# Optimization experiments

Hardware: AMD Instinct MI355X
Metric: run time of the kernel (lower is better)

## Reference

```python
import jax, jax.numpy as jnp
import numpy as np

D_MODEL = 1024
D_STATE = 64
D_CONV = 4
EXPAND = 2
HEADDIM = 64
D_INNER = EXPAND * D_MODEL            # 2048
NHEADS = D_INNER // HEADDIM           # 32
CONV_DIM = D_INNER + 2 * D_STATE      # 2176
D_IN_PROJ = 2 * D_INNER + 2 * D_STATE + NHEADS  # 4256
B, L = 2, 1024


def _mamba2(x, in_proj_w, conv_w, conv_b, dt_bias, A_log, D_param, rms_w, out_proj_w):
    b, l, _ = x.shape
    zxbcdt = x @ in_proj_w.T                                   # (b,l,4256)
    z, xBC, dt = jnp.split(zxbcdt, [D_INNER, D_INNER + CONV_DIM], axis=-1)
    dt = jax.nn.softplus(dt + dt_bias)                         # (b,l,h)
    # depthwise causal conv over sequence
    xBC = jax.lax.conv_general_dilated(
        xBC, conv_w, (1,), [(D_CONV - 1, 0)],
        dimension_numbers=("NLC", "LIO", "NLC"),
        feature_group_count=CONV_DIM) + conv_b
    xBC = jax.nn.silu(xBC)
    xs, Bmat, Cmat = jnp.split(xBC, [D_INNER, D_INNER + D_STATE], axis=-1)
    xh = xs.reshape(b, l, NHEADS, HEADDIM)
    A = -jnp.exp(A_log)                                        # (h,)
    dA = jnp.exp(dt * A)                                       # (b,l,h)

    def step(h, inp):
        dA_t, dt_t, B_t, C_t, x_t = inp                        # (b,h),(b,h),(b,n),(b,n),(b,h,p)
        h = h * dA_t[..., None, None] + (dt_t[..., None] * x_t)[..., None] * B_t[:, None, None, :]
        y_t = jnp.einsum("bhpn,bn->bhp", h, C_t)
        return h, y_t

    h0 = jnp.zeros((b, NHEADS, HEADDIM, D_STATE), x.dtype)
    inps = (dA.transpose(1, 0, 2), dt.transpose(1, 0, 2),
            Bmat.transpose(1, 0, 2), Cmat.transpose(1, 0, 2),
            xh.transpose(1, 0, 2, 3))
    _, ys = jax.lax.scan(step, h0, inps)                       # (l,b,h,p)
    y = ys.transpose(1, 0, 2, 3) + D_param[None, None, :, None] * xh
    y = y.reshape(b, l, D_INNER)
    # gated RMSNorm (norm after gating, as in mamba_ssm RMSNormGated)
    y = y * jax.nn.silu(z)
    y = y * jax.lax.rsqrt(jnp.mean(y * y, axis=-1, keepdims=True) + 1e-5) * rms_w
    return y @ out_proj_w.T


def setup_inputs() -> dict:
    key = jax.random.key(0)
    ks = jax.random.split(key, 16)
    s = 0.02

    def mamba_params(i):
        kk = jax.random.split(ks[i], 8)
        dt = jnp.exp(jax.random.uniform(kk[4], (NHEADS,)) * (np.log(0.1) - np.log(1e-3)) + np.log(1e-3))
        dt_bias = dt + jnp.log(-jnp.expm1(-dt))
        return dict(
            in_proj_w=jax.random.normal(kk[0], (D_IN_PROJ, D_MODEL)) * s,
            conv_w=jax.random.normal(kk[1], (D_CONV, 1, CONV_DIM)) * 0.2,
            conv_b=jnp.zeros((CONV_DIM,)),
            dt_bias=dt_bias,
            A_log=jnp.log(jax.random.uniform(kk[2], (NHEADS,), minval=1.0, maxval=16.0)),
            D=jnp.ones((NHEADS,)),
            rms_w=jnp.ones((D_INNER,)),
            out_proj_w=jax.random.normal(kk[3], (D_MODEL, D_INNER)) * s,
        )

    pf = mamba_params(1)
    pb = mamba_params(2)
    inp = {"x": jax.random.normal(ks[0], (B, L, D_MODEL))}
    for name, v in pf.items():
        inp["f_" + name] = v
    for name, v in pb.items():
        inp["b_" + name] = v
    inp["proj_w"] = jax.random.normal(ks[3], (D_MODEL, 2 * D_MODEL)) * s
    inp["proj_b"] = jnp.zeros((D_MODEL,))
    inp["ln_w"] = jnp.ones((D_MODEL,))
    inp["ln_b"] = jnp.zeros((D_MODEL,))
    return inp


def reference(x, f_in_proj_w, f_conv_w, f_conv_b, f_dt_bias, f_A_log, f_D, f_rms_w, f_out_proj_w,
              b_in_proj_w, b_conv_w, b_conv_b, b_dt_bias, b_A_log, b_D, b_rms_w, b_out_proj_w,
              proj_w, proj_b, ln_w, ln_b):
    out_fwd = _mamba2(x, f_in_proj_w, f_conv_w, f_conv_b, f_dt_bias, f_A_log, f_D, f_rms_w, f_out_proj_w)
    out_bwd = _mamba2(jnp.flip(x, 1), b_in_proj_w, b_conv_w, b_conv_b, b_dt_bias, b_A_log, b_D, b_rms_w, b_out_proj_w)
    out_bwd = jnp.flip(out_bwd, 1)
    combined = jnp.concatenate([out_fwd, out_bwd], axis=-1)
    h = x + combined @ proj_w.T + proj_b
    mu = jnp.mean(h, axis=-1, keepdims=True)
    var = jnp.mean((h - mu) ** 2, axis=-1, keepdims=True)
    return (h - mu) * jax.lax.rsqrt(var + 1e-5) * ln_w + ln_b
```

## Files before the change

kernel.cpp:

```cpp
#include <hip/hip_runtime.h>
#include <hip/hip_bf16.h>

#define DEV __device__ __forceinline__

typedef short bf16x8 __attribute__((ext_vector_type(8)));
typedef float f32x4 __attribute__((ext_vector_type(4)));

static constexpr int BATCH  = 2;
static constexpr int SEQ    = 1024;
static constexpr int DMODEL = 1024;
static constexpr int DINNER = 2048;
static constexpr int DSTATE = 64;
static constexpr int NH     = 32;
static constexpr int HD     = 64;
static constexpr int CONVD  = 2176;
static constexpr int DPROJ  = 4256;
static constexpr int MROWS  = BATCH * SEQ;
static constexpr int NCHUNK = 16;
static constexpr int QC     = 64;

static constexpr size_t OFF_ZX = 0;
static constexpr size_t OFF_XS = OFF_ZX + (size_t)2*MROWS*DPROJ*2;
static constexpr size_t OFF_BB = OFF_XS + (size_t)2*MROWS*DINNER*2;
static constexpr size_t OFF_CC = OFF_BB + (size_t)2*MROWS*DSTATE*4;
static constexpr size_t OFF_DT = OFF_CC + (size_t)2*MROWS*DSTATE*4;
static constexpr size_t OFF_DA = OFF_DT + (size_t)2*MROWS*NH*4;
static constexpr size_t OFF_DR = OFF_DA + (size_t)2*MROWS*NH*4;
static constexpr size_t OFF_CS = OFF_DR + (size_t)2*MROWS*NH*4;
static constexpr size_t OFF_WO = OFF_CS;
static constexpr size_t OFF_WP = OFF_CS + (size_t)2*DMODEL*DINNER*2;
static constexpr size_t OFF_DD = 0;
static constexpr size_t OFF_H  = OFF_DD + (size_t)MROWS*2*DMODEL;

DEV float b2f(ushort u) {
    union { unsigned int i; float f; } v;
    v.i = ((unsigned int)u) << 16;
    return v.f;
}
DEV ushort f2b(float f) {
    union { float f; unsigned int u; } v;
    v.f = f;
    unsigned int r = 0x7FFFu + ((v.u >> 16) & 1u);
    return (ushort)((v.u + r) >> 16);
}
DEV bf16x8 pack8(float4 a, float4 b) {
    bf16x8 r;
    r[0] = (short)f2b(a.x); r[1] = (short)f2b(a.y);
    r[2] = (short)f2b(a.z); r[3] = (short)f2b(a.w);
    r[4] = (short)f2b(b.x); r[5] = (short)f2b(b.y);
    r[6] = (short)f2b(b.z); r[7] = (short)f2b(b.w);
    return r;
}
DEV void gll16(const ushort* g, ushort* l) {
    __builtin_amdgcn_global_load_lds(
        (const __attribute__((address_space(1))) unsigned int*)g,
        (__attribute__((address_space(3))) unsigned int*)l, 16, 0, 0);
}
DEV int idmap128(int bx) {
    int x8 = bx & 7, g = bx >> 3;
    return (x8 & 3) * 32 + (x8 >> 2) * 16 + g;
}

__global__ __launch_bounds__(256) void cvt3_k(
    const float* __restrict__ s0, const float* __restrict__ s1,
    const float* __restrict__ s2,
    ushort* __restrict__ d0, ushort* __restrict__ d1, ushort* __restrict__ d2,
    int b0, int b1)
{
    int blk = blockIdx.x;
    const float* s; ushort* d; size_t off;
    if (blk < b0)            { s = s0; d = d0; off = (size_t)blk * 1024; }
    else if (blk < b0 + b1)  { s = s1; d = d1; off = (size_t)(blk - b0) * 1024; }
    else                     { s = s2; d = d2; off = (size_t)(blk - b0 - b1) * 1024; }
    size_t i = off + threadIdx.x * 4;
    float4 f = *(const float4*)(s + i);
    ushort4 u;
    u.x = f2b(f.x); u.y = f2b(f.y); u.z = f2b(f.z); u.w = f2b(f.w);
    *(ushort4*)(d + i) = u;
}

template<int MODE, int BN, int BK>
__global__ __launch_bounds__(256) void gemm_k(
    const ushort* __restrict__ A, const ushort* __restrict__ W,
    size_t wstride, void* __restrict__ outp, const float* __restrict__ resid,
    const float* __restrict__ bias, float* __restrict__ dtraw,
    int N, int K)
{
    constexpr int BM = 128;
    constexpr int MT = (BN == 128) ? 4 : 2;
    constexpr int NSL = BK / 8;
    constexpr int RPG = 64 / NSL;
    constexpr int NAG = BM / RPG / 4;
    constexpr int NBG = BN / RPG / 4;
    __shared__ ushort As[BM * BK];
    __shared__ ushort Bs[BN * BK];
    const int tid = threadIdx.x;
    const int wave = tid >> 6, lane = tid & 63;
    const int quad = lane >> 4, l16 = lane & 15;
    const int bxu = (MODE == 0)
        ? (int)((blockIdx.x + 2 * blockIdx.y) % gridDim.x) : (int)blockIdx.x;
    const int bn = bxu * BN, bm = blockIdx.y * BM;
    const int dir = blockIdx.z;
    const ushort* Wd = W + (size_t)dir * wstride;
    const int wmoff = (BN == 128) ? (wave >> 1) * 64 : wave * 32;
    const int wnoff = (BN == 128) ? (wave & 1) * 64 : 0;

    const int lrow = lane / NSL, lslot = lane % NSL;
    const ushort* aga[NAG];
    ushort* ald[NAG];
    #pragma unroll
    for (int t = 0; t < NAG; t++) {
        int li = wave * NAG + t;
        int absr = li * RPG + lrow;
        int m = bm + absr;
        size_t rowidx;
        if (MODE == 0) {
            int b = m >> 10, l = m & 1023;
            int ls = dir ? (1023 - l) : l;
            rowidx = (size_t)((b << 10) + ls);
        } else if (MODE == 1) {
            rowidx = (size_t)(dir * MROWS + m);
        } else {
            rowidx = (size_t)m;
        }
        aga[t] = A + rowidx * K + (lslot ^ (absr % NSL)) * 8;
        ald[t] = &As[li * 512];
    }
    const ushort* bga[NBG];
    ushort* bld[NBG];
    #pragma unroll
    for (int t = 0; t < NBG; t++) {
        int li = wave * NBG + t;
        int absr = li * RPG + lrow;
        int n = bn + absr;
        if (n >= N) n = N - 1;
        bga[t] = Wd + (size_t)n * K + (lslot ^ (absr % NSL)) * 8;
        bld[t] = &Bs[li * 512];
    }

    f32x4 acc[MT][4] = {};

    for (int k0 = 0; k0 < K; k0 += BK) {
        #pragma unroll
        for (int t = 0; t < NAG; t++) gll16(aga[t] + k0, ald[t]);
        #pragma unroll
        for (int t = 0; t < NBG; t++) gll16(bga[t] + k0, bld[t]);
        __syncthreads();

        #pragma unroll
        for (int kt = 0; kt < BK / 32; kt++) {
            const int rs = (((kt * 4 + quad) ^ (l16 % NSL))) * 8;
            bf16x8 af[MT], bfr[4];
            #pragma unroll
            for (int mt = 0; mt < MT; mt++)
                af[mt] = *(const bf16x8*)&As[(wmoff + mt * 16 + l16) * BK + rs];
            #pragma unroll
            for (int nt = 0; nt < 4; nt++)
                bfr[nt] = *(const bf16x8*)&Bs[(wnoff + nt * 16 + l16) * BK + rs];
            #pragma unroll
            for (int mt = 0; mt < MT; mt++)
                #pragma unroll
                for (int nt = 0; nt < 4; nt++)
                    acc[mt][nt] = __builtin_amdgcn_mfma_f32_16x16x32_bf16(
                        af[mt], bfr[nt], acc[mt][nt], 0, 0, 0);
        }
        __syncthreads();
    }

    #pragma unroll
    for (int mt = 0; mt < MT; mt++) {
        #pragma unroll
        for (int nt = 0; nt < 4; nt++) {
            #pragma unroll
            for (int j = 0; j < 4; j++) {
                int row = bm + wmoff + mt * 16 + quad * 4 + j;
                int col = bn + wnoff + nt * 16 + l16;
                if (col >= N) continue;
                float v = acc[mt][nt][j];
                if (MODE == 0) {
                    ((ushort*)outp)[(size_t)(dir * MROWS + row) * DPROJ + col] = f2b(v);
                    if (col >= 4224)
                        dtraw[(size_t)(dir * MROWS + row) * NH + (col - 4224)] = v;
                } else if (MODE == 1) {
                    int mr = dir ? ((row & 1024) | (1023 - (row & 1023))) : row;
                    ((ushort*)outp)[(size_t)mr * (2 * DMODEL) + dir * DMODEL + col] = f2b(v);
                } else {
                    float r = resid[(size_t)row * DMODEL + col] + bias[col];
                    ((float*)outp)[(size_t)row * DMODEL + col] = v + r;
                }
            }
        }
    }
}

__global__ __launch_bounds__(256) void conv_k(
    const ushort* __restrict__ zx, const float* __restrict__ dtr,
    const float* __restrict__ cw0, const float* __restrict__ cb0,
    const float* __restrict__ cw1, const float* __restrict__ cb1,
    const float* __restrict__ dtb0, const float* __restrict__ al0,
    const float* __restrict__ dtb1, const float* __restrict__ al1,
    ushort* __restrict__ xs, float* __restrict__ Bq, float* __restrict__ Cq,
    float* __restrict__ dtq, float* __restrict__ ldq)
{
    int bx = blockIdx.x;
    int id = (bx & 7) * 512 + (bx >> 3);
    int dir = id >> 11;
    int m = id & 2047;
    int l = m & 1023;
    const float* cw = dir ? cw1 : cw0;
    const float* cb = dir ? cb1 : cb0;
    int tid = threadIdx.x;

    for (int c = tid * 4; c < CONVD; c += 1024) {
        float4 cbv = *(const float4*)&cb[c];
        float acc[4] = { cbv.x, cbv.y, cbv.z, cbv.w };
        #pragma unroll
        for (int t = 0; t < 4; t++) {
            int ls = l - 3 + t;
            if (ls >= 0) {
                float4 wv = *(const float4*)&cw[t * CONVD + c];
                ushort4 xv = *(const ushort4*)&zx[(size_t)(id - l + ls) * DPROJ + 2048 + c];
                acc[0] += wv.x * b2f(xv.x);
                acc[1] += wv.y * b2f(xv.y);
                acc[2] += wv.z * b2f(xv.z);
                acc[3] += wv.w * b2f(xv.w);
            }
        }
        float v[4];
        #pragma unroll
        for (int i = 0; i < 4; i++) v[i] = acc[i] / (1.f + expf(-acc[i]));
        if (c < DINNER) {
            ushort4 u;
            u.x = f2b(v[0]); u.y = f2b(v[1]); u.z = f2b(v[2]); u.w = f2b(v[3]);
            *(ushort4*)&xs[(size_t)id * DINNER + c] = u;
        } else if (c < DINNER + DSTATE) {
            *(float4*)&Bq[(size_t)id * DSTATE + (c - DINNER)] =
                make_float4(v[0], v[1], v[2], v[3]);
        } else {
            *(float4*)&Cq[(size_t)id * DSTATE + (c - DINNER - DSTATE)] =
                make_float4(v[0], v[1], v[2], v[3]);
        }
    }
    if (tid < NH) {
        const float* dtb = dir ? dtb1 : dtb0;
        const float* al  = dir ? al1 : al0;
        float raw = dtr[(size_t)id * NH + tid] + dtb[tid];
        float dt = raw > 20.f ? raw : log1pf(expf(raw));
        float ldA = -expf(al[tid]) * dt;
        int dirb = id >> 10;
        dtq[(size_t)(dirb * NH + tid) * SEQ + l] = dt;
        ldq[(size_t)(dirb * NH + tid) * SEQ + l] = ldA;
    }
}

__global__ __launch_bounds__(256) void states_k(
    const float* __restrict__ Bq, const float* __restrict__ dtT,
    const float* __restrict__ ldT, const ushort* __restrict__ xsq,
    ushort* __restrict__ cs)
{
    int id = idmap128(blockIdx.x);
    int h = id & 31;
    int c = blockIdx.y;
    int tid = threadIdx.x;
    int wave = tid >> 6, lane = tid & 63;
    int quad = lane >> 4;
    int base = (id >> 5) << 10;
    int l0 = c * QC;

    __shared__ float wsh[QC];
    __shared__ ushort Xw[64][80];
    __shared__ ushort Bt[64][72];

    if (tid < 64) {
        float ld = ldT[(size_t)id * SEQ + l0 + tid];
        #pragma unroll
        for (int st = 1; st < 64; st <<= 1) {
            float o = __shfl_up(ld, st);
            if (tid >= st) ld += o;
        }
        float tot = __shfl(ld, 63);
        wsh[tid] = dtT[(size_t)id * SEQ + l0 + tid] * expf(tot - ld);
    }
    __syncthreads();

    {
        int j = tid >> 2, p0 = (tid & 3) * 16;
        float wj = wsh[j];
        const ushort* xrow = xsq + (size_t)(base + l0 + j) * DINNER + h * HD + p0;
        #pragma unroll
        for (int q = 0; q < 4; q++) {
            ushort4 xv = *(const ushort4*)(xrow + q * 4);
            Xw[p0 + q * 4 + 0][j] = f2b(b2f(xv.x) * wj);
            Xw[p0 + q * 4 + 1][j] = f2b(b2f(xv.y) * wj);
            Xw[p0 + q * 4 + 2][j] = f2b(b2f(xv.z) * wj);
            Xw[p0 + q * 4 + 3][j] = f2b(b2f(xv.w) * wj);
        }
        int j2 = lane, ng = wave * 16;
        const float* brow = Bq + (size_t)(base + l0 + j2) * DSTATE + ng;
        #pragma unroll
        for (int q = 0; q < 4; q++) {
            float4 f = *(const float4*)(brow + q * 4);
            Bt[ng + q * 4 + 0][j2] = f2b(f.x);
            Bt[ng + q * 4 + 1][j2] = f2b(f.y);
            Bt[ng + q * 4 + 2][j2] = f2b(f.z);
            Bt[ng + q * 4 + 3][j2] = f2b(f.w);
        }
    }
    __syncthreads();

    f32x4 acc[4] = {};
    #pragma unroll
    for (int kt = 0; kt < 2; kt++) {
        int k = kt * 32 + quad * 8;
        bf16x8 af = *(const bf16x8*)&Xw[wave * 16 + (lane & 15)][k];
        #pragma unroll
        for (int ni = 0; ni < 4; ni++) {
            bf16x8 bf = *(const bf16x8*)&Bt[ni * 16 + (lane & 15)][k];
            acc[ni] = __builtin_amdgcn_mfma_f32_16x16x32_bf16(af, bf, acc[ni], 0, 0, 0);
        }
    }

    ushort* out = cs + ((size_t)id * NCHUNK + c) * HD * DSTATE;
    #pragma unroll
    for (int ni = 0; ni < 4; ni++) {
        #pragma unroll
        for (int j = 0; j < 4; j++) {
            int p = wave * 16 + quad * 4 + j;
            int n = ni * 16 + (lane & 15);
            out[(size_t)p * DSTATE + n] = f2b(acc[ni][j]);
        }
    }
}

__global__ __launch_bounds__(256) void stitch_k(
    const float* __restrict__ ldT, ushort* __restrict__ cs)
{
    int id = blockIdx.x;
    int tid = threadIdx.x;
    __shared__ float red[256];
    __shared__ float dec[NCHUNK];

    float4 d4 = *(const float4*)(ldT + (size_t)id * SEQ + tid * 4);
    red[tid] = d4.x + d4.y + d4.z + d4.w;
    __syncthreads();
    if (tid < NCHUNK) {
        float s = 0.f;
        #pragma unroll
        for (int i = 0; i < 16; i++) s += red[tid * 16 + i];
        dec[tid] = expf(s);
    }
    __syncthreads();

    int p = tid >> 2, n0 = (tid & 3) * 16;
    ushort* ptr = cs + (size_t)id * NCHUNK * HD * DSTATE + p * DSTATE + n0;

    float st[16];
    #pragma unroll
    for (int i = 0; i < 16; i++) st[i] = 0.f;

    for (int c = 0; c < NCHUNK; c++) {
        ushort* row = ptr + (size_t)c * HD * DSTATE;
        float tmp[16];
        #pragma unroll
        for (int i = 0; i < 16; i++) tmp[i] = b2f(row[i]);
        #pragma unroll
        for (int i = 0; i < 16; i++) row[i] = f2b(st[i]);
        float d = dec[c];
        #pragma unroll
        for (int i = 0; i < 16; i++) st[i] = fmaf(d, st[i], tmp[i]);
    }
}

__global__ __launch_bounds__(256) void ssd_k(
    const float* __restrict__ Bq, const float* __restrict__ Cq,
    const float* __restrict__ dtT, const float* __restrict__ ldT,
    const ushort* __restrict__ xsq, const ushort* __restrict__ cs,
    const float* __restrict__ D0, const float* __restrict__ D1,
    ushort* __restrict__ yout)
{
    int id = idmap128(blockIdx.x);
    int dir = id >> 6, h = id & 31;
    int c = blockIdx.y;
    int tid = threadIdx.x;
    int wave = tid >> 6, lane = tid & 63;
    int quad = lane >> 4;
    int base = (id >> 5) << 10;
    int l0 = c * QC;

    __shared__ float cum[QC], dts[QC];
    __shared__ ushort Ms[64][72];
    __shared__ ushort Xb[64][80];

    {
        int j = tid >> 2, p0 = (tid & 3) * 16;
        const ushort* xrow = xsq + (size_t)(base + l0 + j) * DINNER + h * HD + p0;
        #pragma unroll
        for (int q = 0; q < 4; q++) {
            ushort4 xv = *(const ushort4*)(xrow + q * 4);
            Xb[p0 + q * 4 + 0][j] = xv.x;
            Xb[p0 + q * 4 + 1][j] = xv.y;
            Xb[p0 + q * 4 + 2][j] = xv.z;
            Xb[p0 + q * 4 + 3][j] = xv.w;
        }
    }
    if (tid < 64) {
        float ld = ldT[(size_t)id * SEQ + l0 + tid];
        #pragma unroll
        for (int st = 1; st < 64; st <<= 1) {
            float o = __shfl_up(ld, st);
            if (tid >= st) ld += o;
        }
        cum[tid] = ld;
        dts[tid] = dtT[(size_t)id * SEQ + l0 + tid];
    }

    f32x4 sacc[4] = {};
    #pragma unroll
    for (int kt = 0; kt < 2; kt++) {
        int k = kt * 32 + quad * 8;
        const float* cp = Cq + (size_t)(base + l0 + wave * 16 + (lane & 15)) * DSTATE + k;
        bf16x8 af = pack8(*(const float4*)cp, *(const float4*)(cp + 4));
        #pragma unroll
        for (int ni = 0; ni < 4; ni++) {
            const float* bp = Bq + (size_t)(base + l0 + ni * 16 + (lane & 15)) * DSTATE + k;
            bf16x8 bf = pack8(*(const float4*)bp, *(const float4*)(bp + 4));
            sacc[ni] = __builtin_amdgcn_mfma_f32_16x16x32_bf16(af, bf, sacc[ni], 0, 0, 0);
        }
    }
    __syncthreads();

    #pragma unroll
    for (int ni = 0; ni < 4; ni++) {
        int j = ni * 16 + (lane & 15);
        float cj = cum[j], dj = dts[j];
        #pragma unroll
        for (int r = 0; r < 4; r++) {
            int l = wave * 16 + quad * 4 + r;
            float v = 0.f;
            if (l >= j) v = expf(cum[l] - cj) * dj * sacc[ni][r];
            Ms[l][j] = f2b(v);
        }
    }
    __syncthreads();

    f32x4 acc[4] = {};
    #pragma unroll
    for (int kt = 0; kt < 2; kt++) {
        int k = kt * 32 + quad * 8;
        bf16x8 af = *(const bf16x8*)&Ms[wave * 16 + (lane & 15)][k];
        #pragma unroll
        for (int ni = 0; ni < 4; ni++) {
            bf16x8 bf = *(const bf16x8*)&Xb[ni * 16 + (lane & 15)][k];
            acc[ni] = __builtin_amdgcn_mfma_f32_16x16x32_bf16(af, bf, acc[ni], 0, 0, 0);
        }
    }
    const ushort* Hrow = cs + ((size_t)id * NCHUNK + c) * HD * DSTATE;
    {
        float cl = expf(cum[wave * 16 + (lane & 15)]);
        #pragma unroll
        for (int kt = 0; kt < 2; kt++) {
            int k = kt * 32 + quad * 8;
            const float* cp = Cq + (size_t)(base + l0 + wave * 16 + (lane & 15)) * DSTATE + k;
            float4 c0 = *(const float4*)cp;
            float4 c1 = *(const float4*)(cp + 4);
            float4 s0 = {c0.x * cl, c0.y * cl, c0.z * cl, c0.w * cl};
            float4 s1 = {c1.x * cl, c1.y * cl, c1.z * cl, c1.w * cl};
            bf16x8 af = pack8(s0, s1);
            #pragma unroll
            for (int ni = 0; ni < 4; ni++) {
                bf16x8 bf = *(const bf16x8*)(Hrow + (size_t)(ni * 16 + (lane & 15)) * DSTATE + k);
                acc[ni] = __builtin_amdgcn_mfma_f32_16x16x32_bf16(af, bf, acc[ni], 0, 0, 0);
            }
        }
    }

    float Dv = (dir ? D1 : D0)[h];
    int lb = wave * 16 + quad * 4;
    #pragma unroll
    for (int ni = 0; ni < 4; ni++) {
        int p = ni * 16 + (lane & 15);
        ushort4 x4 = *(const ushort4*)&Xb[p][lb];
        float xv[4] = { b2f(x4.x), b2f(x4.y), b2f(x4.z), b2f(x4.w) };
        #pragma unroll
        for (int r = 0; r < 4; r++) {
            int l = lb + r;
            yout[(size_t)(base + l0 + l) * DPROJ + 2048 + h * HD + p] =
                f2b(acc[ni][r] + Dv * xv[r]);
        }
    }
}

__global__ __launch_bounds__(256) void grms_cvt_k(
    const ushort* __restrict__ zx,
    const float* __restrict__ rw0, const float* __restrict__ rw1,
    ushort* __restrict__ yn,
    const float* __restrict__ fow, const float* __restrict__ bow,
    const float* __restrict__ pw,
    ushort* __restrict__ wo, ushort* __restrict__ wp)
{
    int blk = blockIdx.x;
    int tid = threadIdx.x;
    if (blk >= 4096) {
        int b = blk - 4096;
        const float* s; ushort* d; size_t off;
        if (b < 2048)      { s = fow; d = wo;                           off = (size_t)b * 1024; }
        else if (b < 4096) { s = bow; d = wo + (size_t)DMODEL * DINNER; off = (size_t)(b - 2048) * 1024; }
        else               { s = pw;  d = wp;                           off = (size_t)(b - 4096) * 1024; }
        size_t i = off + tid * 4;
        float4 f = *(const float4*)(s + i);
        ushort4 u;
        u.x = f2b(f.x); u.y = f2b(f.y); u.z = f2b(f.z); u.w = f2b(f.w);
        *(ushort4*)(d + i) = u;
        return;
    }
    int id = blk;
    int dir = id >> 11;
    const float* rw = dir ? rw1 : rw0;
    int c0 = tid * 8;
    ushort zv[8], yv[8];
    *(uint4*)zv = *(const uint4*)&zx[(size_t)id * DPROJ + c0];
    *(uint4*)yv = *(const uint4*)&zx[(size_t)id * DPROJ + 2048 + c0];
    float g[8];
    float ss = 0.f;
    #pragma unroll
    for (int i = 0; i < 8; i++) {
        float z = b2f(zv[i]);
        float v = b2f(yv[i]) * (z / (1.f + expf(-z)));
        g[i] = v;
        ss += v * v;
    }
    for (int o = 32; o; o >>= 1) ss += __shfl_down(ss, o);
    __shared__ float t4[4];
    if ((tid & 63) == 0) t4[tid >> 6] = ss;
    __syncthreads();
    ss = t4[0] + t4[1] + t4[2] + t4[3];
    float sc = rsqrtf(ss * (1.f / DINNER) + 1e-5f);
    ushort u[8];
    #pragma unroll
    for (int i = 0; i < 8; i++) u[i] = f2b(g[i] * sc * rw[c0 + i]);
    *(uint4*)&yn[(size_t)id * DINNER + c0] = *(uint4*)u;
}

__global__ __launch_bounds__(256) void ln_k(
    const float* __restrict__ h, const float* __restrict__ lw,
    const float* __restrict__ lb, float* __restrict__ out)
{
    int m = blockIdx.x;
    int tid = threadIdx.x;
    int c = tid * 4;
    float4 v = *(const float4*)&h[(size_t)m * DMODEL + c];
    float s  = v.x + v.y + v.z + v.w;
    float s2 = v.x * v.x + v.y * v.y + v.z * v.z + v.w * v.w;
    for (int o = 32; o; o >>= 1) { s += __shfl_down(s, o); s2 += __shfl_down(s2, o); }
    __shared__ float ts[4], ts2[4];
    if ((tid & 63) == 0) { ts[tid >> 6] = s; ts2[tid >> 6] = s2; }
    __syncthreads();
    s  = ts[0] + ts[1] + ts[2] + ts[3];
    s2 = ts2[0] + ts2[1] + ts2[2] + ts2[3];
    float mu  = s * (1.f / DMODEL);
    float var = s2 * (1.f / DMODEL) - mu * mu;
    float sc  = rsqrtf(var + 1e-5f);
    float4 w4 = *(const float4*)&lw[c];
    float4 b4 = *(const float4*)&lb[c];
    float4 o4;
    o4.x = (v.x - mu) * sc * w4.x + b4.x;
    o4.y = (v.y - mu) * sc * w4.y + b4.y;
    o4.z = (v.z - mu) * sc * w4.z + b4.z;
    o4.w = (v.w - mu) * sc * w4.w + b4.w;
    *(float4*)&out[(size_t)m * DMODEL + c] = o4;
}

extern "C" void kernel_launch(void* const* d_in, const int* in_sizes, int n_in,
                              void* d_out, int out_size, void* d_ws, size_t ws_size,
                              hipStream_t stream)
{
    const float* x     = (const float*)d_in[0];
    const float* f_inw = (const float*)d_in[1];
    const float* f_cw  = (const float*)d_in[2];
    const float* f_cb  = (const float*)d_in[3];
    const float* f_dtb = (const float*)d_in[4];
    const float* f_al  = (const float*)d_in[5];
    const float* f_Dp  = (const float*)d_in[6];
    const float* f_rw  = (const float*)d_in[7];
    const float* f_ow  = (const float*)d_in[8];
    const float* b_inw = (const float*)d_in[9];
    const float* b_cw  = (const float*)d_in[10];
    const float* b_cb  = (const float*)d_in[11];
    const float* b_dtb = (const float*)d_in[12];
    const float* b_al  = (const float*)d_in[13];
    const float* b_Dp  = (const float*)d_in[14];
    const float* b_rw  = (const float*)d_in[15];
    const float* b_ow  = (const float*)d_in[16];
    const float* projw = (const float*)d_in[17];
    const float* projb = (const float*)d_in[18];
    const float* lnw   = (const float*)d_in[19];
    const float* lnb   = (const float*)d_in[20];

    char* ws = (char*)d_ws;
    ushort* zx  = (ushort*)(ws + OFF_ZX);
    ushort* xs  = (ushort*)(ws + OFF_XS);
    float*  Bq  = (float*)(ws + OFF_BB);
    float*  Cq  = (float*)(ws + OFF_CC);
    float*  dtq = (float*)(ws + OFF_DT);
    float*  ldq = (float*)(ws + OFF_DA);
    float*  dtr = (float*)(ws + OFF_DR);
    ushort* wbf = (ushort*)(ws + OFF_CS);
    ushort* cs  = (ushort*)(ws + OFF_CS);
    ushort* xbf = (ushort*)(ws + OFF_XS);
    ushort* yn  = (ushort*)(ws + OFF_XS);
    ushort* dd  = (ushort*)(ws + OFF_DD);
    float*  hb  = (float*)(ws + OFF_H);
    ushort* wo  = (ushort*)(ws + OFF_WO);
    ushort* wp  = (ushort*)(ws + OFF_WP);

    cvt3_k<<<dim3(2 * DPROJ + MROWS), 256, 0, stream>>>(
        f_inw, b_inw, x, wbf, wbf + (size_t)DPROJ * DMODEL, xbf, DPROJ, DPROJ);

    gemm_k<0, 128, 64><<<dim3((DPROJ + 127) / 128, MROWS / 128, 2), 256, 0, stream>>>(
        xbf, wbf, (size_t)DPROJ * DMODEL, (void*)zx, nullptr, nullptr, dtr,
        DPROJ, DMODEL);

    conv_k<<<dim3(2 * MROWS), 256, 0, stream>>>(
        zx, dtr, f_cw, f_cb, b_cw, b_cb, f_dtb, f_al, b_dtb, b_al,
        xs, Bq, Cq, dtq, ldq);

    states_k<<<dim3(128, NCHUNK), 256, 0, stream>>>(Bq, dtq, ldq, xs, cs);
    stitch_k<<<dim3(128), 256, 0, stream>>>(ldq, cs);
    ssd_k<<<dim3(128, NCHUNK), 256, 0, stream>>>(
        Bq, Cq, dtq, ldq, xs, cs, f_Dp, b_Dp, zx);

    grms_cvt_k<<<dim3(4096 + 3 * MROWS), 256, 0, stream>>>(
        zx, f_rw, b_rw, yn, f_ow, b_ow, projw, wo, wp);

    gemm_k<1, 64, 128><<<dim3(DMODEL / 64, MROWS / 128, 2), 256, 0, stream>>>(
        yn, wo, (size_t)DMODEL * DINNER, (void*)dd, nullptr, nullptr, nullptr,
        DMODEL, DINNER);

    gemm_k<2, 64, 128><<<dim3(DMODEL / 64, MROWS / 128, 1), 256, 0, stream>>>(
        dd, wp, 0, (void*)hb, x, projb, nullptr, DMODEL, DINNER);

    ln_k<<<dim3(MROWS), 256, 0, stream>>>(hb, lnw, lnb, (float*)d_out);
}
```

Before: 347.3 us.

## Double-buffer GEMM LDS loads with vmcnt waits and retile the in-projection GEMM

Replaces the single-buffered GEMM with a double-buffered pipeline. Asynchronous global-to-LDS loads for the next K-step are issued while MFMAs run on the current buffer, and waits use explicit vmcnt counts and raw barriers. The in-projection GEMM moves to 256x128 tiles with 512 threads and BK=32. The output GEMMs go to BK=64. This is meant to hide global load latency behind compute, in exchange for twice the LDS and fragile hand-written wait counts.

```diff
diff --git a/kernel.cpp b/kernel.cpp
--- a/kernel.cpp
+++ b/kernel.cpp
@@ -56,6 +56,15 @@
         (const __attribute__((address_space(1))) unsigned int*)g,
         (__attribute__((address_space(3))) unsigned int*)l, 16, 0, 0);
 }
+template<int N> DEV void waitv() {
+    if constexpr (N == 0) asm volatile("s_waitcnt vmcnt(0)" ::: "memory");
+    else if constexpr (N == 3) asm volatile("s_waitcnt vmcnt(3)" ::: "memory");
+    else if constexpr (N == 6) asm volatile("s_waitcnt vmcnt(6)" ::: "memory");
+}
+DEV void barrier_raw() {
+    __builtin_amdgcn_sched_barrier(0);
+    asm volatile("s_barrier" ::: "memory");
+}
 DEV int idmap128(int bx) {
     int x8 = bx & 7, g = bx >> 3;
     return (x8 & 3) * 32 + (x8 >> 2) * 16 + g;
@@ -79,21 +88,29 @@
     *(ushort4*)(d + i) = u;
 }
 
-template<int MODE, int BN, int BK>
-__global__ __launch_bounds__(256) void gemm_k(
+template<int MODE, int BM, int BN, int BK, int NTHR>
+__global__ __launch_bounds__(NTHR) void gemm_pipe_k(
     const ushort* __restrict__ A, const ushort* __restrict__ W,
     size_t wstride, void* __restrict__ outp, const float* __restrict__ resid,
     const float* __restrict__ bias, float* __restrict__ dtraw,
     int N, int K)
 {
-    constexpr int BM = 128;
-    constexpr int MT = (BN == 128) ? 4 : 2;
-    constexpr int NSL = BK / 8;
-    constexpr int RPG = 64 / NSL;
-    constexpr int NAG = BM / RPG / 4;
-    constexpr int NBG = BN / RPG / 4;
-    __shared__ ushort As[BM * BK];
-    __shared__ ushort Bs[BN * BK];
+    constexpr int NW   = NTHR / 64;
+    constexpr int NSL  = BK / 8;
+    constexpr int RPG  = 64 / NSL;
+    constexpr int NAG  = BM / RPG / NW;
+    constexpr int NBG  = BN / RPG / NW;
+    constexpr int NGLL = NAG + NBG;
+    constexpr int WNW  = BN / 64;
+    constexpr int WMN  = NW / WNW;
+    constexpr int WMS  = BM / WMN;
+    constexpr int MT   = WMS / 16;
+    static_assert(NGLL == 3 || NGLL == 6, "vmcnt literal");
+    static_assert(BN % 64 == 0 && BM % (RPG * NW) == 0, "geometry");
+
+    __shared__ ushort As[2][BM * BK];
+    __shared__ ushort Bs[2][BN * BK];
+
     const int tid = threadIdx.x;
     const int wave = tid >> 6, lane = tid & 63;
     const int quad = lane >> 4, l16 = lane & 15;
@@ -102,12 +119,12 @@
     const int bn = bxu * BN, bm = blockIdx.y * BM;
     const int dir = blockIdx.z;
     const ushort* Wd = W + (size_t)dir * wstride;
-    const int wmoff = (BN == 128) ? (wave >> 1) * 64 : wave * 32;
-    const int wnoff = (BN == 128) ? (wave & 1) * 64 : 0;
+    const int wmoff = (wave / WNW) * WMS;
+    const int wnoff = (wave % WNW) * 64;
 
     const int lrow = lane / NSL, lslot = lane % NSL;
     const ushort* aga[NAG];
-    ushort* ald[NAG];
+    int ald[NAG];
     #pragma unroll
     for (int t = 0; t < NAG; t++) {
         int li = wave * NAG + t;
@@ -123,40 +140,42 @@
         } else {
             rowidx = (size_t)m;
         }
-        aga[t] = A + rowidx * K + (lslot ^ (absr % NSL)) * 8;
-        ald[t] = &As[li * 512];
+        aga[t] = A + rowidx * K + (lslot ^ (absr & (NSL - 1))) * 8;
+        ald[t] = li * 512;
     }
     const ushort* bga[NBG];
-    ushort* bld[NBG];
+    int bld[NBG];
     #pragma unroll
     for (int t = 0; t < NBG; t++) {
         int li = wave * NBG + t;
         int absr = li * RPG + lrow;
         int n = bn + absr;
         if (n >= N) n = N - 1;
-        bga[t] = Wd + (size_t)n * K + (lslot ^ (absr % NSL)) * 8;
-        bld[t] = &Bs[li * 512];
-    }
-
+        bga[t] = Wd + (size_t)n * K + (lslot ^ (absr & (NSL - 1))) * 8;
+        bld[t] = li * 512;
+    }
+
+    const int NSTEP = K / BK;
     f32x4 acc[MT][4] = {};
 
-    for (int k0 = 0; k0 < K; k0 += BK) {
-        #pragma unroll
-        for (int t = 0; t < NAG; t++) gll16(aga[t] + k0, ald[t]);
-        #pragma unroll
-        for (int t = 0; t < NBG; t++) gll16(bga[t] + k0, bld[t]);
-        __syncthreads();
-
+    auto STAGE = [&](int buf, int step) {
+        const int k0 = step * BK;
+        #pragma unroll
+        for (int t = 0; t < NAG; t++) gll16(aga[t] + k0, &As[buf][ald[t]]);
+        #pragma unroll
+        for (int t = 0; t < NBG; t++) gll16(bga[t] + k0, &Bs[buf][bld[t]]);
+    };
+    auto COMPUTE = [&](int buf) {
         #pragma unroll
         for (int kt = 0; kt < BK / 32; kt++) {
-            const int rs = (((kt * 4 + quad) ^ (l16 % NSL))) * 8;
+            const int rs = ((kt * 4 + quad) ^ (l16 & (NSL - 1))) * 8;
             bf16x8 af[MT], bfr[4];
             #pragma unroll
             for (int mt = 0; mt < MT; mt++)
-                af[mt] = *(const bf16x8*)&As[(wmoff + mt * 16 + l16) * BK + rs];
+                af[mt] = *(const bf16x8*)&As[buf][(wmoff + mt * 16 + l16) * BK + rs];
             #pragma unroll
             for (int nt = 0; nt < 4; nt++)
-                bfr[nt] = *(const bf16x8*)&Bs[(wnoff + nt * 16 + l16) * BK + rs];
+                bfr[nt] = *(const bf16x8*)&Bs[buf][(wnoff + nt * 16 + l16) * BK + rs];
             #pragma unroll
             for (int mt = 0; mt < MT; mt++)
                 #pragma unroll
@@ -164,7 +183,24 @@
                     acc[mt][nt] = __builtin_amdgcn_mfma_f32_16x16x32_bf16(
                         af[mt], bfr[nt], acc[mt][nt], 0, 0, 0);
         }
-        __syncthreads();
+    };
+
+    STAGE(0, 0);
+    STAGE(1, 1);
+    waitv<NGLL>();
+    barrier_raw();
+
+    for (int t = 0; t < NSTEP; t += 2) {
+        COMPUTE(0);
+        barrier_raw();
+        if (t + 2 < NSTEP) { STAGE(0, t + 2); waitv<NGLL>(); }
+        else               { waitv<0>(); }
+        barrier_raw();
+        COMPUTE(1);
+        barrier_raw();
+        if (t + 3 < NSTEP) { STAGE(1, t + 3); waitv<NGLL>(); }
+        else               { waitv<0>(); }
+        barrier_raw();
     }
 
     #pragma unroll
@@ -616,7 +652,8 @@
     cvt3_k<<<dim3(2 * DPROJ + MROWS), 256, 0, stream>>>(
         f_inw, b_inw, x, wbf, wbf + (size_t)DPROJ * DMODEL, xbf, DPROJ, DPROJ);
 
-    gemm_k<0, 128, 64><<<dim3((DPROJ + 127) / 128, MROWS / 128, 2), 256, 0, stream>>>(
+    gemm_pipe_k<0, 256, 128, 32, 512>
+        <<<dim3((DPROJ + 127) / 128, MROWS / 256, 2), 512, 0, stream>>>(
         xbf, wbf, (size_t)DPROJ * DMODEL, (void*)zx, nullptr, nullptr, dtr,
         DPROJ, DMODEL);
 
@@ -632,11 +669,13 @@
     grms_cvt_k<<<dim3(4096 + 3 * MROWS), 256, 0, stream>>>(
         zx, f_rw, b_rw, yn, f_ow, b_ow, projw, wo, wp);
 
-    gemm_k<1, 64, 128><<<dim3(DMODEL / 64, MROWS / 128, 2), 256, 0, stream>>>(
+    gemm_pipe_k<1, 128, 64, 64, 256>
+        <<<dim3(DMODEL / 64, MROWS / 128, 2), 256, 0, stream>>>(
         yn, wo, (size_t)DMODEL * DINNER, (void*)dd, nullptr, nullptr, nullptr,
         DMODEL, DINNER);
 
-    gemm_k<2, 64, 128><<<dim3(DMODEL / 64, MROWS / 128, 1), 256, 0, stream>>>(
+    gemm_pipe_k<2, 128, 64, 64, 256>
+        <<<dim3(DMODEL / 64, MROWS / 128, 1), 256, 0, stream>>>(
         dd, wp, 0, (void*)hb, x, projb, nullptr, DMODEL, DINNER);
 
     ln_k<<<dim3(MROWS), 256, 0, stream>>>(hb, lnw, lnb, (float*)d_out);
```

Result: no change. 354.0 us (+1.9%).
